# Kernel optimization log

Measured on AMD Instinct MI355X. Metric: run time of the kernel, lower is better.

Reference implementation:

```python
import jax, jax.numpy as jnp
import numpy as np

IN_FEATURES = 4096
OUT_FEATURES = 11008
GROUP_SIZE = 128
NBITS = 4
ALPHA = 0.05  # relative noise scale: sigma = ALPHA * |w|


def setup_inputs() -> dict:
    key = jax.random.key(0)
    k_x, k_q, k_s, k_z, k_b, k_n = jax.random.split(key, 6)
    n_groups = IN_FEATURES // GROUP_SIZE  # 32
    x = jax.random.normal(k_x, (4096, IN_FEATURES), dtype=jnp.float32)
    qweight = jax.random.randint(k_q, (OUT_FEATURES, IN_FEATURES), 0, 2 ** NBITS, dtype=jnp.int32)
    scales = jax.random.uniform(k_s, (OUT_FEATURES, n_groups), dtype=jnp.float32) * 0.01 + 1e-4
    zeros = jax.random.uniform(k_z, (OUT_FEATURES, n_groups), dtype=jnp.float32) * (2 ** NBITS)
    bias = jax.random.normal(k_b, (OUT_FEATURES,), dtype=jnp.float32)
    noise = jax.random.normal(k_n, (OUT_FEATURES, IN_FEATURES), dtype=jnp.float32)
    return {"x": x, "qweight": qweight, "scales": scales, "zeros": zeros, "bias": bias, "noise": noise}


def _dequantize(qweight, scales, zeros):
    # grouped dequant: w[o, g*G + j] = (q - zero[o,g]) * scale[o,g]
    out_f, in_f = qweight.shape
    n_groups = scales.shape[1]
    qg = qweight.reshape(out_f, n_groups, GROUP_SIZE).astype(scales.dtype)
    w = (qg - zeros[:, :, None]) * scales[:, :, None]
    return w.reshape(out_f, in_f)


def reference(x, qweight, scales, zeros, bias, noise):
    w = _dequantize(qweight, scales, zeros)[:, :IN_FEATURES]
    sigma = ALPHA * jnp.abs(w)            # noise_fn(weight, alpha)
    w_noisy = (w + noise * sigma).astype(x.dtype)
    # F.linear: x @ w.T + bias
    return jnp.einsum('bi,oi->bo', x, w_noisy) + bias
```

## Files before the change

kernel.cpp:

```cpp
#include <hip/hip_runtime.h>
#include <hip/hip_bf16.h>
#include <stdint.h>

#define M_ROWS 4096
#define IN_F   4096
#define OUT_F  11008
#define N_GROUPS 32
#define ALPHA  0.05f

typedef __bf16 bf16;
typedef __bf16 bf16x8 __attribute__((ext_vector_type(8)));
typedef float  floatx4 __attribute__((ext_vector_type(4)));

__device__ __forceinline__ void async_copy16(const void* g, void* l) {
  __builtin_amdgcn_global_load_lds(
      (const __attribute__((address_space(1))) void*)g,
      (__attribute__((address_space(3))) void*)l, 16, 0, 0);
}

__global__ __launch_bounds__(256) void dequant_noise_kernel(
    const int* __restrict__ q, const float* __restrict__ scales,
    const float* __restrict__ zeros, const float* __restrict__ noise,
    bf16* __restrict__ wn) {
  int gid = blockIdx.x * 256 + threadIdx.x;
  int o = gid >> 9;
  int i = (gid & 511) << 3;
  int g = i >> 7;
  float s = scales[o * N_GROUPS + g];
  float z = zeros[o * N_GROUPS + g];
  size_t base = (size_t)o * IN_F + i;
  int4   q0 = *(const int4*)(q + base);
  int4   q1 = *(const int4*)(q + base + 4);
  float4 n0 = *(const float4*)(noise + base);
  float4 n1 = *(const float4*)(noise + base + 4);
  float qs[8] = {(float)q0.x, (float)q0.y, (float)q0.z, (float)q0.w,
                 (float)q1.x, (float)q1.y, (float)q1.z, (float)q1.w};
  float ns[8] = {n0.x, n0.y, n0.z, n0.w, n1.x, n1.y, n1.z, n1.w};
  bf16x8 out;
#pragma unroll
  for (int j = 0; j < 8; ++j) {
    float w = (qs[j] - z) * s;
    float v = fmaf(ALPHA * fabsf(w), ns[j], w);
    out[j] = (bf16)v;
  }
  *(bf16x8*)(wn + base) = out;
}

__global__ __launch_bounds__(256) void xcast_kernel(
    const float* __restrict__ x, bf16* __restrict__ xb) {
  size_t base = ((size_t)blockIdx.x * 256 + threadIdx.x) << 3;
  float4 a0 = *(const float4*)(x + base);
  float4 a1 = *(const float4*)(x + base + 4);
  float vs[8] = {a0.x, a0.y, a0.z, a0.w, a1.x, a1.y, a1.z, a1.w};
  bf16x8 out;
#pragma unroll
  for (int j = 0; j < 8; ++j) out[j] = (bf16)vs[j];
  *(bf16x8*)(xb + base) = out;
}

#define NH (IN_F / 32)

__global__ __launch_bounds__(512, 2) void gemm_8ph_kernel(
    const bf16* __restrict__ A,
    const bf16* __restrict__ W,
    const float* __restrict__ bias,
    float* __restrict__ C) {
  __shared__ bf16 lds[4 * 16384];

  const int tid = threadIdx.x;
  const int wv = tid >> 6;
  const int ln = tid & 63;
  const int wr = wv >> 2;
  const int wc = wv & 3;

  const int orig = blockIdx.x;
  const int idx  = orig >> 3;
  const int bm   = ((orig & 7) << 1) | (idx & 1);
  const int bn   = idx >> 1;
  const int mbase = bm << 8;
  const int nbase = bn << 8;

  const int dec    = (ln & 7) ^ (ln >> 3);
  const int rstage = wv * 32 + (ln >> 3) * 2 + (dec >> 2);
  const int kcol   = (dec & 3) * 8;
  const bf16* aS = A + (size_t)(mbase + rstage) * IN_F + kcol;
  const bf16* bS = W + (size_t)(nbase + rstage) * IN_F + kcol;

  const int frow = ln & 15;
  const int g4   = ln >> 4;
  const int pc   = (((frow & 1) << 2) | g4) ^ (frow >> 1);
  const int aoff = (wr * 64 + (frow >> 1)) * 64 + pc * 8;
  const int boff = 8192 + (wc * 32 + (frow >> 1)) * 64 + pc * 8;

  floatx4 acc[8][4] = {};

#define STAGE_A(DST, KH)                                                          \
  do {                                                                            \
    async_copy16(aS + (size_t)(KH) * 32,             &lds[(DST) * 16384 + wv * 1024]);        \
    async_copy16(aS + (size_t)(KH) * 32 + 16 * IN_F, &lds[(DST) * 16384 + wv * 1024 + 512]);  \
  } while (0)
#define STAGE_B(DST, KH)                                                          \
  do {                                                                            \
    async_copy16(bS + (size_t)(KH) * 32,             &lds[(DST) * 16384 + 8192 + wv * 1024]);       \
    async_copy16(bS + (size_t)(KH) * 32 + 16 * IN_F, &lds[(DST) * 16384 + 8192 + wv * 1024 + 512]); \
  } while (0)

  STAGE_A(0, 0); STAGE_B(0, 0);
  STAGE_A(1, 1); STAGE_B(1, 1);
  STAGE_A(2, 2); STAGE_B(2, 2);
  asm volatile("s_waitcnt vmcnt(8)" ::: "memory");
  __builtin_amdgcn_s_barrier();

#define PAIR(SLOT, KH, DO_STAGE, TVM)                                             \
  {                                                                               \
    bf16x8 afr[4], bfr[4], afr2[4];                                               \
    _Pragma("unroll") for (int mi = 0; mi < 4; ++mi)                              \
      afr[mi] = *(const bf16x8*)&lds[(SLOT) * 16384 + aoff + mi * 512];           \
    _Pragma("unroll") for (int ni = 0; ni < 4; ++ni)                              \
      bfr[ni] = *(const bf16x8*)&lds[(SLOT) * 16384 + boff + ni * 512];           \
    if (DO_STAGE) STAGE_A(((SLOT) + 3) & 3, (KH) + 3);                            \
    __builtin_amdgcn_s_barrier();                                                 \
    asm volatile("s_waitcnt lgkmcnt(0)" ::: "memory");                            \
    __builtin_amdgcn_s_setprio(1);                                                \
    _Pragma("unroll") for (int mi = 0; mi < 4; ++mi)                              \
      _Pragma("unroll") for (int ni = 0; ni < 4; ++ni)                            \
        acc[mi][ni] = __builtin_amdgcn_mfma_f32_16x16x32_bf16(                    \
            afr[mi], bfr[ni], acc[mi][ni], 0, 0, 0);                              \
    __builtin_amdgcn_s_setprio(0);                                                \
    __builtin_amdgcn_s_barrier();                                                 \
    _Pragma("unroll") for (int mi = 0; mi < 4; ++mi)                              \
      afr2[mi] = *(const bf16x8*)&lds[(SLOT) * 16384 + aoff + (4 + mi) * 512];    \
    if (DO_STAGE) STAGE_B(((SLOT) + 3) & 3, (KH) + 3);                            \
    __builtin_amdgcn_s_barrier();                                                 \
    asm volatile("s_waitcnt lgkmcnt(0)" ::: "memory");                            \
    __builtin_amdgcn_s_setprio(1);                                                \
    _Pragma("unroll") for (int mi = 0; mi < 4; ++mi)                              \
      _Pragma("unroll") for (int ni = 0; ni < 4; ++ni)                            \
        acc[4 + mi][ni] = __builtin_amdgcn_mfma_f32_16x16x32_bf16(                \
            afr2[mi], bfr[ni], acc[4 + mi][ni], 0, 0, 0);                         \
    __builtin_amdgcn_s_setprio(0);                                                \
    asm volatile("s_waitcnt " TVM ::: "memory");                                  \
    __builtin_amdgcn_s_barrier();                                                 \
  }

  for (int kh = 0; kh < 124; kh += 4) {
    PAIR(0, kh + 0, true, "vmcnt(8)");
    PAIR(1, kh + 1, true, "vmcnt(8)");
    PAIR(2, kh + 2, true, "vmcnt(8)");
    PAIR(3, kh + 3, true, "vmcnt(8)");
  }
  PAIR(0, 124, true,  "vmcnt(8)");
  PAIR(1, 125, false, "vmcnt(4)");
  PAIR(2, 126, false, "vmcnt(0)");
  PAIR(3, 127, false, "vmcnt(0)");

#undef PAIR
#undef STAGE_A
#undef STAGE_B

#pragma unroll
  for (int ni = 0; ni < 4; ++ni) {
    int n = nbase + wc * 64 + ni * 16 + (ln & 15);
    float bv = bias[n];
#pragma unroll
    for (int mi = 0; mi < 8; ++mi) {
      int m0 = mbase + wr * 128 + mi * 16 + (ln >> 4) * 4;
#pragma unroll
      for (int r = 0; r < 4; ++r)
        C[(size_t)(m0 + r) * OUT_F + n] = acc[mi][ni][r] + bv;
    }
  }
}

extern "C" void kernel_launch(void* const* d_in, const int* in_sizes, int n_in,
                              void* d_out, int out_size, void* d_ws, size_t ws_size,
                              hipStream_t stream) {
  const float* x       = (const float*)d_in[0];
  const int*   qweight = (const int*)d_in[1];
  const float* scales  = (const float*)d_in[2];
  const float* zeros   = (const float*)d_in[3];
  const float* bias    = (const float*)d_in[4];
  const float* noise   = (const float*)d_in[5];
  float* out = (float*)d_out;

  bf16* wn = (bf16*)d_ws;
  bf16* xb = (bf16*)((char*)d_ws + (size_t)OUT_F * IN_F * sizeof(bf16));

  dequant_noise_kernel<<<(OUT_F * (IN_F / 8)) / 256, 256, 0, stream>>>(
      qweight, scales, zeros, noise, wn);
  xcast_kernel<<<(M_ROWS * (IN_F / 8)) / 256, 256, 0, stream>>>(x, xb);

  gemm_8ph_kernel<<<dim3(688), 512, 0, stream>>>(xb, wn, bias, out);
}
```

Baseline: 774.7 us.

## Switch GEMM to 32x32x16 MFMA tiles and fuse prep kernels

The GEMM inner loop now uses 32x32x16 bf16 MFMA instructions with 16-wide accumulators, in place of 16x16x32. Fragment addressing and the epilogue store pattern change to match. Each phase now reads fewer LDS fragments per MFMA, and the larger instruction may run at higher throughput. Separately, the dequant/noise kernel and the x cast kernel are merged into one grid-stride prep kernel, which saves a launch. The risks are a wrong LDS swizzle or fragment layout for the new MFMA shape, and a more scattered output store pattern.

Result: slower. 795.9 us (+2.7%).

```diff
diff --git a/kernel.cpp b/kernel.cpp
--- a/kernel.cpp
+++ b/kernel.cpp
@@ -10,7 +10,7 @@
 
 typedef __bf16 bf16;
 typedef __bf16 bf16x8 __attribute__((ext_vector_type(8)));
-typedef float  floatx4 __attribute__((ext_vector_type(4)));
+typedef float  floatx16 __attribute__((ext_vector_type(16)));
 
 __device__ __forceinline__ void async_copy16(const void* g, void* l) {
   __builtin_amdgcn_global_load_lds(
@@ -18,47 +18,49 @@
       (__attribute__((address_space(3))) void*)l, 16, 0, 0);
 }
 
-__global__ __launch_bounds__(256) void dequant_noise_kernel(
-    const int* __restrict__ q, const float* __restrict__ scales,
-    const float* __restrict__ zeros, const float* __restrict__ noise,
-    bf16* __restrict__ wn) {
-  int gid = blockIdx.x * 256 + threadIdx.x;
-  int o = gid >> 9;
-  int i = (gid & 511) << 3;
-  int g = i >> 7;
-  float s = scales[o * N_GROUPS + g];
-  float z = zeros[o * N_GROUPS + g];
-  size_t base = (size_t)o * IN_F + i;
-  int4   q0 = *(const int4*)(q + base);
-  int4   q1 = *(const int4*)(q + base + 4);
-  float4 n0 = *(const float4*)(noise + base);
-  float4 n1 = *(const float4*)(noise + base + 4);
-  float qs[8] = {(float)q0.x, (float)q0.y, (float)q0.z, (float)q0.w,
-                 (float)q1.x, (float)q1.y, (float)q1.z, (float)q1.w};
-  float ns[8] = {n0.x, n0.y, n0.z, n0.w, n1.x, n1.y, n1.z, n1.w};
-  bf16x8 out;
+__global__ __launch_bounds__(256) void prep_kernel(
+    const float* __restrict__ x, const int* __restrict__ q,
+    const float* __restrict__ scales, const float* __restrict__ zeros,
+    const float* __restrict__ noise, bf16* __restrict__ wn,
+    bf16* __restrict__ xb) {
+  const int W_CH = OUT_F * (IN_F >> 3);
+  const int T_CH = W_CH + (M_ROWS * (IN_F >> 3));
+  const int stride = gridDim.x * 256;
+  for (int idx = blockIdx.x * 256 + threadIdx.x; idx < T_CH; idx += stride) {
+    if (idx < W_CH) {
+      int o = idx >> 9;
+      int i = (idx & 511) << 3;
+      int g = i >> 7;
+      float s = scales[o * N_GROUPS + g];
+      float z = zeros[o * N_GROUPS + g];
+      size_t base = (size_t)o * IN_F + i;
+      int4   q0 = *(const int4*)(q + base);
+      int4   q1 = *(const int4*)(q + base + 4);
+      float4 n0 = *(const float4*)(noise + base);
+      float4 n1 = *(const float4*)(noise + base + 4);
+      float qs[8] = {(float)q0.x, (float)q0.y, (float)q0.z, (float)q0.w,
+                     (float)q1.x, (float)q1.y, (float)q1.z, (float)q1.w};
+      float ns[8] = {n0.x, n0.y, n0.z, n0.w, n1.x, n1.y, n1.z, n1.w};
+      bf16x8 outv;
 #pragma unroll
-  for (int j = 0; j < 8; ++j) {
-    float w = (qs[j] - z) * s;
-    float v = fmaf(ALPHA * fabsf(w), ns[j], w);
-    out[j] = (bf16)v;
+      for (int j = 0; j < 8; ++j) {
+        float w = (qs[j] - z) * s;
+        float v = fmaf(ALPHA * fabsf(w), ns[j], w);
+        outv[j] = (bf16)v;
+      }
+      *(bf16x8*)(wn + base) = outv;
+    } else {
+      size_t base = (size_t)(idx - W_CH) << 3;
+      float4 a0 = *(const float4*)(x + base);
+      float4 a1 = *(const float4*)(x + base + 4);
+      float vs[8] = {a0.x, a0.y, a0.z, a0.w, a1.x, a1.y, a1.z, a1.w};
+      bf16x8 outv;
+#pragma unroll
+      for (int j = 0; j < 8; ++j) outv[j] = (bf16)vs[j];
+      *(bf16x8*)(xb + base) = outv;
+    }
   }
-  *(bf16x8*)(wn + base) = out;
 }
-
-__global__ __launch_bounds__(256) void xcast_kernel(
-    const float* __restrict__ x, bf16* __restrict__ xb) {
-  size_t base = ((size_t)blockIdx.x * 256 + threadIdx.x) << 3;
-  float4 a0 = *(const float4*)(x + base);
-  float4 a1 = *(const float4*)(x + base + 4);
-  float vs[8] = {a0.x, a0.y, a0.z, a0.w, a1.x, a1.y, a1.z, a1.w};
-  bf16x8 out;
-#pragma unroll
-  for (int j = 0; j < 8; ++j) out[j] = (bf16)vs[j];
-  *(bf16x8*)(xb + base) = out;
-}
-
-#define NH (IN_F / 32)
 
 __global__ __launch_bounds__(512, 2) void gemm_8ph_kernel(
     const bf16* __restrict__ A,
@@ -86,13 +88,13 @@
   const bf16* aS = A + (size_t)(mbase + rstage) * IN_F + kcol;
   const bf16* bS = W + (size_t)(nbase + rstage) * IN_F + kcol;
 
-  const int frow = ln & 15;
-  const int g4   = ln >> 4;
-  const int pc   = (((frow & 1) << 2) | g4) ^ (frow >> 1);
-  const int aoff = (wr * 64 + (frow >> 1)) * 64 + pc * 8;
-  const int boff = 8192 + (wc * 32 + (frow >> 1)) * 64 + pc * 8;
+  const int l31 = ln & 31;
+  const int g2  = ln >> 5;
+  const int pc  = (((ln & 1) << 2) | g2) ^ ((l31 >> 1) & 7);
+  const int aoff0 =        (wr * 64 + (l31 >> 1)) * 64 + pc * 8;
+  const int boff0 = 8192 + (wc * 32 + (l31 >> 1)) * 64 + pc * 8;
 
-  floatx4 acc[8][4] = {};
+  floatx16 acc[4][2] = {};
 
 #define STAGE_A(DST, KH)                                                          \
   do {                                                                            \
@@ -113,31 +115,33 @@
 
 #define PAIR(SLOT, KH, DO_STAGE, TVM)                                             \
   {                                                                               \
-    bf16x8 afr[4], bfr[4], afr2[4];                                               \
-    _Pragma("unroll") for (int mi = 0; mi < 4; ++mi)                              \
-      afr[mi] = *(const bf16x8*)&lds[(SLOT) * 16384 + aoff + mi * 512];           \
-    _Pragma("unroll") for (int ni = 0; ni < 4; ++ni)                              \
-      bfr[ni] = *(const bf16x8*)&lds[(SLOT) * 16384 + boff + ni * 512];           \
+    bf16x8 af[4], bq[2];                                                          \
+    _Pragma("unroll") for (int mt = 0; mt < 4; ++mt)                              \
+      af[mt] = *(const bf16x8*)&lds[(SLOT) * 16384 + aoff0 + mt * 1024];          \
+    _Pragma("unroll") for (int nt = 0; nt < 2; ++nt)                              \
+      bq[nt] = *(const bf16x8*)&lds[(SLOT) * 16384 + boff0 + nt * 1024];          \
     if (DO_STAGE) STAGE_A(((SLOT) + 3) & 3, (KH) + 3);                            \
     __builtin_amdgcn_s_barrier();                                                 \
     asm volatile("s_waitcnt lgkmcnt(0)" ::: "memory");                            \
     __builtin_amdgcn_s_setprio(1);                                                \
-    _Pragma("unroll") for (int mi = 0; mi < 4; ++mi)                              \
-      _Pragma("unroll") for (int ni = 0; ni < 4; ++ni)                            \
-        acc[mi][ni] = __builtin_amdgcn_mfma_f32_16x16x32_bf16(                    \
-            afr[mi], bfr[ni], acc[mi][ni], 0, 0, 0);                              \
+    _Pragma("unroll") for (int mt = 0; mt < 4; ++mt)                              \
+      _Pragma("unroll") for (int nt = 0; nt < 2; ++nt)                            \
+        acc[mt][nt] = __builtin_amdgcn_mfma_f32_32x32x16_bf16(                    \
+            af[mt], bq[nt], acc[mt][nt], 0, 0, 0);                                \
     __builtin_amdgcn_s_setprio(0);                                                \
     __builtin_amdgcn_s_barrier();                                                 \
-    _Pragma("unroll") for (int mi = 0; mi < 4; ++mi)                              \
-      afr2[mi] = *(const bf16x8*)&lds[(SLOT) * 16384 + aoff + (4 + mi) * 512];    \
+    _Pragma("unroll") for (int mt = 0; mt < 4; ++mt)                              \
+      af[mt] = *(const bf16x8*)&lds[(SLOT) * 16384 + ((aoff0 ^ 16) + mt * 1024)]; \
+    _Pragma("unroll") for (int nt = 0; nt < 2; ++nt)                              \
+      bq[nt] = *(const bf16x8*)&lds[(SLOT) * 16384 + ((boff0 ^ 16) + nt * 1024)]; \
     if (DO_STAGE) STAGE_B(((SLOT) + 3) & 3, (KH) + 3);                            \
     __builtin_amdgcn_s_barrier();                                                 \
     asm volatile("s_waitcnt lgkmcnt(0)" ::: "memory");                            \
     __builtin_amdgcn_s_setprio(1);                                                \
-    _Pragma("unroll") for (int mi = 0; mi < 4; ++mi)                              \
-      _Pragma("unroll") for (int ni = 0; ni < 4; ++ni)                            \
-        acc[4 + mi][ni] = __builtin_amdgcn_mfma_f32_16x16x32_bf16(                \
-            afr2[mi], bfr[ni], acc[4 + mi][ni], 0, 0, 0);                         \
+    _Pragma("unroll") for (int mt = 0; mt < 4; ++mt)                              \
+      _Pragma("unroll") for (int nt = 0; nt < 2; ++nt)                            \
+        acc[mt][nt] = __builtin_amdgcn_mfma_f32_32x32x16_bf16(                    \
+            af[mt], bq[nt], acc[mt][nt], 0, 0, 0);                                \
     __builtin_amdgcn_s_setprio(0);                                                \
     asm volatile("s_waitcnt " TVM ::: "memory");                                  \
     __builtin_amdgcn_s_barrier();                                                 \
@@ -159,15 +163,17 @@
 #undef STAGE_B
 
 #pragma unroll
-  for (int ni = 0; ni < 4; ++ni) {
-    int n = nbase + wc * 64 + ni * 16 + (ln & 15);
+  for (int nt = 0; nt < 2; ++nt) {
+    int n = nbase + wc * 64 + nt * 32 + l31;
     float bv = bias[n];
 #pragma unroll
-    for (int mi = 0; mi < 8; ++mi) {
-      int m0 = mbase + wr * 128 + mi * 16 + (ln >> 4) * 4;
+    for (int mt = 0; mt < 4; ++mt) {
+      int mb2 = mbase + wr * 128 + mt * 32 + 4 * g2;
 #pragma unroll
-      for (int r = 0; r < 4; ++r)
-        C[(size_t)(m0 + r) * OUT_F + n] = acc[mi][ni][r] + bv;
+      for (int r = 0; r < 16; ++r) {
+        int m = mb2 + (r & 3) + 8 * (r >> 2);
+        C[(size_t)m * OUT_F + n] = acc[mt][nt][r] + bv;
+      }
     }
   }
 }
@@ -186,9 +192,7 @@
   bf16* wn = (bf16*)d_ws;
   bf16* xb = (bf16*)((char*)d_ws + (size_t)OUT_F * IN_F * sizeof(bf16));
 
-  dequant_noise_kernel<<<(OUT_F * (IN_F / 8)) / 256, 256, 0, stream>>>(
-      qweight, scales, zeros, noise, wn);
-  xcast_kernel<<<(M_ROWS * (IN_F / 8)) / 256, 256, 0, stream>>>(x, xb);
+  prep_kernel<<<2048, 256, 0, stream>>>(x, qweight, scales, zeros, noise, wn, xb);
 
   gemm_8ph_kernel<<<dim3(688), 512, 0, stream>>>(xb, wn, bias, out);
 }
```

## Merge prep kernels and drop intra-step barriers in GEMM pipeline

Applied to the files above, without the earlier changes.

Fuses the dequant+noise and x-cast kernels into one grid-stride prep kernel, which saves a launch and the gap between kernels. In the GEMM main loop it removes two of the three workgroup barriers and the explicit lgkmcnt waits inside each k-step, keeping one barrier per step and adding sched_barrier fences. This cuts synchronisation stalls. Removing the barriers between a stage issue and the LDS reads risks correctness if the slot being overwritten is still being read, though the four-slot ring with a three-step lookahead is meant to keep that safe.

Result: no change. 781.3 us (+0.9%).

```diff
diff --git a/kernel.cpp b/kernel.cpp
--- a/kernel.cpp
+++ b/kernel.cpp
@@ -18,47 +18,49 @@
       (__attribute__((address_space(3))) void*)l, 16, 0, 0);
 }
 
-__global__ __launch_bounds__(256) void dequant_noise_kernel(
-    const int* __restrict__ q, const float* __restrict__ scales,
-    const float* __restrict__ zeros, const float* __restrict__ noise,
-    bf16* __restrict__ wn) {
-  int gid = blockIdx.x * 256 + threadIdx.x;
-  int o = gid >> 9;
-  int i = (gid & 511) << 3;
-  int g = i >> 7;
-  float s = scales[o * N_GROUPS + g];
-  float z = zeros[o * N_GROUPS + g];
-  size_t base = (size_t)o * IN_F + i;
-  int4   q0 = *(const int4*)(q + base);
-  int4   q1 = *(const int4*)(q + base + 4);
-  float4 n0 = *(const float4*)(noise + base);
-  float4 n1 = *(const float4*)(noise + base + 4);
-  float qs[8] = {(float)q0.x, (float)q0.y, (float)q0.z, (float)q0.w,
-                 (float)q1.x, (float)q1.y, (float)q1.z, (float)q1.w};
-  float ns[8] = {n0.x, n0.y, n0.z, n0.w, n1.x, n1.y, n1.z, n1.w};
-  bf16x8 out;
+__global__ __launch_bounds__(256) void prep_kernel(
+    const float* __restrict__ x, const int* __restrict__ q,
+    const float* __restrict__ scales, const float* __restrict__ zeros,
+    const float* __restrict__ noise, bf16* __restrict__ wn,
+    bf16* __restrict__ xb) {
+  const int W_CH = OUT_F * (IN_F >> 3);
+  const int T_CH = W_CH + (M_ROWS * (IN_F >> 3));
+  const int stride = gridDim.x * 256;
+  for (int idx = blockIdx.x * 256 + threadIdx.x; idx < T_CH; idx += stride) {
+    if (idx < W_CH) {
+      int o = idx >> 9;
+      int i = (idx & 511) << 3;
+      int g = i >> 7;
+      float s = scales[o * N_GROUPS + g];
+      float z = zeros[o * N_GROUPS + g];
+      size_t base = (size_t)o * IN_F + i;
+      int4   q0 = *(const int4*)(q + base);
+      int4   q1 = *(const int4*)(q + base + 4);
+      float4 n0 = *(const float4*)(noise + base);
+      float4 n1 = *(const float4*)(noise + base + 4);
+      float qs[8] = {(float)q0.x, (float)q0.y, (float)q0.z, (float)q0.w,
+                     (float)q1.x, (float)q1.y, (float)q1.z, (float)q1.w};
+      float ns[8] = {n0.x, n0.y, n0.z, n0.w, n1.x, n1.y, n1.z, n1.w};
+      bf16x8 outv;
 #pragma unroll
-  for (int j = 0; j < 8; ++j) {
-    float w = (qs[j] - z) * s;
-    float v = fmaf(ALPHA * fabsf(w), ns[j], w);
-    out[j] = (bf16)v;
+      for (int j = 0; j < 8; ++j) {
+        float w = (qs[j] - z) * s;
+        float v = fmaf(ALPHA * fabsf(w), ns[j], w);
+        outv[j] = (bf16)v;
+      }
+      *(bf16x8*)(wn + base) = outv;
+    } else {
+      size_t base = (size_t)(idx - W_CH) << 3;
+      float4 a0 = *(const float4*)(x + base);
+      float4 a1 = *(const float4*)(x + base + 4);
+      float vs[8] = {a0.x, a0.y, a0.z, a0.w, a1.x, a1.y, a1.z, a1.w};
+      bf16x8 outv;
+#pragma unroll
+      for (int j = 0; j < 8; ++j) outv[j] = (bf16)vs[j];
+      *(bf16x8*)(xb + base) = outv;
+    }
   }
-  *(bf16x8*)(wn + base) = out;
 }
-
-__global__ __launch_bounds__(256) void xcast_kernel(
-    const float* __restrict__ x, bf16* __restrict__ xb) {
-  size_t base = ((size_t)blockIdx.x * 256 + threadIdx.x) << 3;
-  float4 a0 = *(const float4*)(x + base);
-  float4 a1 = *(const float4*)(x + base + 4);
-  float vs[8] = {a0.x, a0.y, a0.z, a0.w, a1.x, a1.y, a1.z, a1.w};
-  bf16x8 out;
-#pragma unroll
-  for (int j = 0; j < 8; ++j) out[j] = (bf16)vs[j];
-  *(bf16x8*)(xb + base) = out;
-}
-
-#define NH (IN_F / 32)
 
 __global__ __launch_bounds__(512, 2) void gemm_8ph_kernel(
     const bf16* __restrict__ A,
@@ -89,7 +91,7 @@
   const int frow = ln & 15;
   const int g4   = ln >> 4;
   const int pc   = (((frow & 1) << 2) | g4) ^ (frow >> 1);
-  const int aoff = (wr * 64 + (frow >> 1)) * 64 + pc * 8;
+  const int aoff =        (wr * 64 + (frow >> 1)) * 64 + pc * 8;
   const int boff = 8192 + (wc * 32 + (frow >> 1)) * 64 + pc * 8;
 
   floatx4 acc[8][4] = {};
@@ -110,6 +112,7 @@
   STAGE_A(2, 2); STAGE_B(2, 2);
   asm volatile("s_waitcnt vmcnt(8)" ::: "memory");
   __builtin_amdgcn_s_barrier();
+  __builtin_amdgcn_sched_barrier(0);
 
 #define PAIR(SLOT, KH, DO_STAGE, TVM)                                             \
   {                                                                               \
@@ -119,20 +122,15 @@
     _Pragma("unroll") for (int ni = 0; ni < 4; ++ni)                              \
       bfr[ni] = *(const bf16x8*)&lds[(SLOT) * 16384 + boff + ni * 512];           \
     if (DO_STAGE) STAGE_A(((SLOT) + 3) & 3, (KH) + 3);                            \
-    __builtin_amdgcn_s_barrier();                                                 \
-    asm volatile("s_waitcnt lgkmcnt(0)" ::: "memory");                            \
     __builtin_amdgcn_s_setprio(1);                                                \
     _Pragma("unroll") for (int mi = 0; mi < 4; ++mi)                              \
       _Pragma("unroll") for (int ni = 0; ni < 4; ++ni)                            \
         acc[mi][ni] = __builtin_amdgcn_mfma_f32_16x16x32_bf16(                    \
             afr[mi], bfr[ni], acc[mi][ni], 0, 0, 0);                              \
     __builtin_amdgcn_s_setprio(0);                                                \
-    __builtin_amdgcn_s_barrier();                                                 \
     _Pragma("unroll") for (int mi = 0; mi < 4; ++mi)                              \
       afr2[mi] = *(const bf16x8*)&lds[(SLOT) * 16384 + aoff + (4 + mi) * 512];    \
     if (DO_STAGE) STAGE_B(((SLOT) + 3) & 3, (KH) + 3);                            \
-    __builtin_amdgcn_s_barrier();                                                 \
-    asm volatile("s_waitcnt lgkmcnt(0)" ::: "memory");                            \
     __builtin_amdgcn_s_setprio(1);                                                \
     _Pragma("unroll") for (int mi = 0; mi < 4; ++mi)                              \
       _Pragma("unroll") for (int ni = 0; ni < 4; ++ni)                            \
@@ -141,6 +139,7 @@
     __builtin_amdgcn_s_setprio(0);                                                \
     asm volatile("s_waitcnt " TVM ::: "memory");                                  \
     __builtin_amdgcn_s_barrier();                                                 \
+    __builtin_amdgcn_sched_barrier(0);                                            \
   }
 
   for (int kh = 0; kh < 124; kh += 4) {
@@ -186,9 +185,7 @@
   bf16* wn = (bf16*)d_ws;
   bf16* xb = (bf16*)((char*)d_ws + (size_t)OUT_F * IN_F * sizeof(bf16));
 
-  dequant_noise_kernel<<<(OUT_F * (IN_F / 8)) / 256, 256, 0, stream>>>(
-      qweight, scales, zeros, noise, wn);
-  xcast_kernel<<<(M_ROWS * (IN_F / 8)) / 256, 256, 0, stream>>>(x, xb);
+  prep_kernel<<<2048, 256, 0, stream>>>(x, qweight, scales, zeros, noise, wn, xb);
 
   gemm_8ph_kernel<<<dim3(688), 512, 0, stream>>>(xb, wn, bias, out);
 }
```
